# Optimization experiments

Measured on AMD Instinct MI355X. Metric: run time of the kernel, lower is better.

The kernel has to match this reference:

```python
import jax, jax.numpy as jnp
from jax import lax
import numpy as np

N_INPUTS = 256
N_REGS = 256
BATCH = 4096
T = 64  # num_clk_cycles


def setup_inputs() -> dict:
    key = jax.random.key(0)
    k1, k2, k3 = jax.random.split(key, 3)
    P = jax.random.normal(k1, (N_INPUTS, BATCH, T), dtype=jnp.float32)
    wa = jax.random.randint(k2, (N_REGS,), 0, N_INPUTS + N_REGS, dtype=jnp.int32)
    wb = jax.random.randint(k3, (N_REGS,), 0, N_INPUTS + N_REGS, dtype=jnp.int32)
    return {"P": P, "wa": wa, "wb": wb}


def reference(P, wa, wb):
    # PIEmbedding: clamp params to [-2,2], sigmoid(4*param[:, idx]) per cycle.
    # Precompute all cycles at once: X[t, b, i] in (0,1).
    X = jax.nn.sigmoid(4.0 * jnp.clip(P, -2.0, 2.0))          # [n_inputs, B, T]
    X = jnp.transpose(X, (2, 1, 0))                            # [T, B, n_inputs]
    B = P.shape[1]

    # Representative exec-generated soft sequential circuit:
    # each of N_REGS gates is a soft XOR of two signals drawn from
    # concat([primary_inputs, registers]); gate outputs become next registers.
    def step(states, x_t):
        sig = jnp.concatenate([x_t, states], axis=-1)          # [B, n_inputs+n_regs]
        a = sig[:, wa]                                          # [B, n_regs]
        b = sig[:, wb]
        new_states = a + b - 2.0 * a * b                        # soft XOR
        return new_states, None

    init = jnp.full((B, N_REGS), 0.5, dtype=P.dtype)            # init_registers()
    out, _ = lax.scan(step, init, X)                            # scan over clk cycles
    return out                                                  # [B, n_regs]
```

## Files before the change

### kernel.cpp

```cpp
#include <hip/hip_runtime.h>

#define N_IN   256
#define N_REG  256
#define NBATCH 4096
#define TT     64
#define TC     16
#define NCHUNK (TT / TC)
#define XT_LD  17
#define ST_BASE (N_IN * XT_LD)

__global__ __launch_bounds__(64, 2) void circuit_scan(
    const float* __restrict__ P,
    const int*   __restrict__ wa,
    const int*   __restrict__ wb,
    float*       __restrict__ out)
{
    __shared__ float lds[ST_BASE + N_REG];

    const int lane = threadIdx.x;
    const int b    = blockIdx.x;
    const float* Pb = P + (size_t)b * TT;

    const float* pa0[4]; const float* pb0[4];
    int inca[4], incb[4];
    float sv[4];

    #pragma unroll
    for (int k = 0; k < 4; ++k) {
        const int r  = lane + 64 * k;
        const int ia = wa[r];
        const int ib = wb[r];
        const bool axk = ia < N_IN;
        const bool bxk = ib < N_IN;
        pa0[k] = lds + (axk ? ia * XT_LD : ST_BASE + (ia - N_IN));
        pb0[k] = lds + (bxk ? ib * XT_LD : ST_BASE + (ib - N_IN));
        inca[k] = axk ? 1 : 0;
        incb[k] = bxk ? 1 : 0;
        lds[ST_BASE + r] = 0.5f;
        sv[k] = 0.5f;
    }

    float4 pf[16];
    #pragma unroll
    for (int k2 = 0; k2 < 4; ++k2) {
        const size_t rbase = (size_t)(lane + 64 * k2) * ((size_t)NBATCH * TT);
        #pragma unroll
        for (int q = 0; q < 4; ++q)
            pf[k2 * 4 + q] = *reinterpret_cast<const float4*>(Pb + rbase + q * 4);
    }

    for (int c = 0; c < NCHUNK; ++c) {
        #pragma unroll
        for (int k2 = 0; k2 < 4; ++k2) {
            const int r = lane + 64 * k2;
            #pragma unroll
            for (int q = 0; q < 4; ++q) {
                const float4 v = pf[k2 * 4 + q];
                const float xs[4] = {v.x, v.y, v.z, v.w};
                #pragma unroll
                for (int j = 0; j < 4; ++j) {
                    float x = fminf(2.0f, fmaxf(-2.0f, xs[j]));
                    lds[r * XT_LD + 4 * q + j] = 1.0f / (1.0f + __expf(-4.0f * x));
                }
            }
        }
        if (c + 1 < NCHUNK) {
            #pragma unroll
            for (int k2 = 0; k2 < 4; ++k2) {
                const size_t rbase = (size_t)(lane + 64 * k2) * ((size_t)NBATCH * TT);
                #pragma unroll
                for (int q = 0; q < 4; ++q)
                    pf[k2 * 4 + q] = *reinterpret_cast<const float4*>(
                        Pb + rbase + (c + 1) * TC + q * 4);
            }
        }
        const float* pa[4]; const float* pb[4];
        #pragma unroll
        for (int k = 0; k < 4; ++k) { pa[k] = pa0[k]; pb[k] = pb0[k]; }

        #pragma unroll
        for (int t = 0; t < TC; ++t) {
            float av[4], bv[4];
            #pragma unroll
            for (int k = 0; k < 4; ++k) { av[k] = *pa[k]; bv[k] = *pb[k]; }
            #pragma unroll
            for (int k = 0; k < 4; ++k) {
                const float a  = av[k];
                const float bb = bv[k];
                const float ns = a + bb - 2.0f * a * bb;
                sv[k] = ns;
                lds[ST_BASE + lane + 64 * k] = ns;
                pa[k] += inca[k];
                pb[k] += incb[k];
            }
        }
    }

    #pragma unroll
    for (int k = 0; k < 4; ++k)
        out[(size_t)b * N_REG + lane + 64 * k] = sv[k];
}

extern "C" void kernel_launch(void* const* d_in, const int* in_sizes, int n_in,
                              void* d_out, int out_size, void* d_ws, size_t ws_size,
                              hipStream_t stream) {
    const float* P   = (const float*)d_in[0];
    const int*   wa  = (const int*)d_in[1];
    const int*   wb  = (const int*)d_in[2];
    float*       out = (float*)d_out;
    circuit_scan<<<NBATCH, 64, 0, stream>>>(P, wa, wb, out);
}
```

Baseline: 388.8 us.

## Precompute sigmoid and transpose inputs in a separate kernel before the scan

Adds a tiled transpose kernel that applies clamp+sigmoid and writes X in [batch][t][input] layout to workspace. The scan kernel then loads contiguous float4 rows per timestep, with a smaller time chunk and higher occupancy bound. This removes the transcendental work and strided loads from the latency-bound scan. The cost is an extra full read+write pass over a large intermediate buffer and a reliance on workspace size.

```diff
diff --git a/kernel.cpp b/kernel.cpp
--- a/kernel.cpp
+++ b/kernel.cpp
@@ -4,13 +4,50 @@
 #define N_REG  256
 #define NBATCH 4096
 #define TT     64
-#define TC     16
+#define PLANE  ((size_t)NBATCH * TT)
+#define TC     8
 #define NCHUNK (TT / TC)
-#define XT_LD  17
-#define ST_BASE (N_IN * XT_LD)
+#define ST_BASE (TC * N_IN)
 
-__global__ __launch_bounds__(64, 2) void circuit_scan(
-    const float* __restrict__ P,
+__global__ __launch_bounds__(256) void sig_transpose(
+    const float* __restrict__ P, float* __restrict__ Xt)
+{
+    __shared__ float tile[64][65];
+    const int tid  = threadIdx.x;
+    const int rt   = blockIdx.x & 3;
+    const size_t ct = blockIdx.x >> 2;
+    const int r0   = rt * 64;
+    const size_t c0 = ct * 64;
+    const int col4 = (tid & 15) * 4;
+    const int row  = tid >> 4;
+
+    #pragma unroll
+    for (int i = 0; i < 4; ++i) {
+        const int ri = row + 16 * i;
+        const float4 v = *reinterpret_cast<const float4*>(
+            P + (size_t)(r0 + ri) * PLANE + c0 + col4);
+        const float xs[4] = {v.x, v.y, v.z, v.w};
+        #pragma unroll
+        for (int j = 0; j < 4; ++j) {
+            float x = fminf(2.0f, fmaxf(-2.0f, xs[j]));
+            tile[ri][col4 + j] = 1.0f / (1.0f + __expf(-4.0f * x));
+        }
+    }
+    __syncthreads();
+    #pragma unroll
+    for (int i = 0; i < 4; ++i) {
+        const int ci = row + 16 * i;
+        float4 w;
+        w.x = tile[col4 + 0][ci];
+        w.y = tile[col4 + 1][ci];
+        w.z = tile[col4 + 2][ci];
+        w.w = tile[col4 + 3][ci];
+        *reinterpret_cast<float4*>(Xt + (c0 + ci) * 256 + r0 + col4) = w;
+    }
+}
+
+__global__ __launch_bounds__(64, 4) void circuit_scan(
+    const float* __restrict__ Xt,
     const int*   __restrict__ wa,
     const int*   __restrict__ wb,
     float*       __restrict__ out)
@@ -19,7 +56,7 @@
 
     const int lane = threadIdx.x;
     const int b    = blockIdx.x;
-    const float* Pb = P + (size_t)b * TT;
+    const float* Xb = Xt + (size_t)b * (TT * N_IN);
 
     const float* pa0[4]; const float* pb0[4];
     int inca[4], incb[4];
@@ -30,49 +67,30 @@
         const int r  = lane + 64 * k;
         const int ia = wa[r];
         const int ib = wb[r];
-        const bool axk = ia < N_IN;
-        const bool bxk = ib < N_IN;
-        pa0[k] = lds + (axk ? ia * XT_LD : ST_BASE + (ia - N_IN));
-        pb0[k] = lds + (bxk ? ib * XT_LD : ST_BASE + (ib - N_IN));
-        inca[k] = axk ? 1 : 0;
-        incb[k] = bxk ? 1 : 0;
+        const bool ax = ia < N_IN;
+        const bool bx = ib < N_IN;
+        pa0[k] = lds + (ax ? ia : ST_BASE + (ia - N_IN));
+        pb0[k] = lds + (bx ? ib : ST_BASE + (ib - N_IN));
+        inca[k] = ax ? N_IN : 0;
+        incb[k] = bx ? N_IN : 0;
         lds[ST_BASE + r] = 0.5f;
         sv[k] = 0.5f;
     }
 
-    float4 pf[16];
+    float4 pf[TC];
     #pragma unroll
-    for (int k2 = 0; k2 < 4; ++k2) {
-        const size_t rbase = (size_t)(lane + 64 * k2) * ((size_t)NBATCH * TT);
-        #pragma unroll
-        for (int q = 0; q < 4; ++q)
-            pf[k2 * 4 + q] = *reinterpret_cast<const float4*>(Pb + rbase + q * 4);
-    }
+    for (int t = 0; t < TC; ++t)
+        pf[t] = *reinterpret_cast<const float4*>(Xb + (size_t)t * N_IN + lane * 4);
 
     for (int c = 0; c < NCHUNK; ++c) {
         #pragma unroll
-        for (int k2 = 0; k2 < 4; ++k2) {
-            const int r = lane + 64 * k2;
-            #pragma unroll
-            for (int q = 0; q < 4; ++q) {
-                const float4 v = pf[k2 * 4 + q];
-                const float xs[4] = {v.x, v.y, v.z, v.w};
-                #pragma unroll
-                for (int j = 0; j < 4; ++j) {
-                    float x = fminf(2.0f, fmaxf(-2.0f, xs[j]));
-                    lds[r * XT_LD + 4 * q + j] = 1.0f / (1.0f + __expf(-4.0f * x));
-                }
-            }
-        }
+        for (int t = 0; t < TC; ++t)
+            *reinterpret_cast<float4*>(&lds[t * N_IN + lane * 4]) = pf[t];
         if (c + 1 < NCHUNK) {
             #pragma unroll
-            for (int k2 = 0; k2 < 4; ++k2) {
-                const size_t rbase = (size_t)(lane + 64 * k2) * ((size_t)NBATCH * TT);
-                #pragma unroll
-                for (int q = 0; q < 4; ++q)
-                    pf[k2 * 4 + q] = *reinterpret_cast<const float4*>(
-                        Pb + rbase + (c + 1) * TC + q * 4);
-            }
+            for (int t = 0; t < TC; ++t)
+                pf[t] = *reinterpret_cast<const float4*>(
+                    Xb + (size_t)((c + 1) * TC + t) * N_IN + lane * 4);
         }
         const float* pa[4]; const float* pb[4];
         #pragma unroll
@@ -108,5 +126,8 @@
     const int*   wa  = (const int*)d_in[1];
     const int*   wb  = (const int*)d_in[2];
     float*       out = (float*)d_out;
-    circuit_scan<<<NBATCH, 64, 0, stream>>>(P, wa, wb, out);
+    float*       Xt  = (float*)d_ws;
+
+    sig_transpose<<<16384, 256, 0, stream>>>(P, Xt);
+    circuit_scan<<<NBATCH, 64, 0, stream>>>(Xt, wa, wb, out);
 }
```

Measured after the change: 508.1 us. +30.7%, slower.
